# Performance work log

Hardware: AMD Instinct MI355X
Metric: run time of the kernel (lower is better)

Reference implementation:

```python
import jax, jax.numpy as jnp
from jax import lax
import numpy as np

BN_EPS = 1e-5


def setup_inputs() -> dict:
    key = jax.random.key(0)
    ks = jax.random.split(key, 10)
    B, S, I, H, O = 256, 2048, 64, 128, 1
    return {
        "x": jax.random.normal(ks[0], (B, S, I), dtype=jnp.float32),
        "mask": jax.random.randint(ks[1], (B, S, I), 0, 2, dtype=jnp.int32),
        "delta": jax.random.uniform(ks[2], (B, S, I), dtype=jnp.float32),
        "x_mean": jax.random.normal(ks[3], (I,), dtype=jnp.float32),
        "w_ih": jax.random.normal(ks[4], (3 * H, I), dtype=jnp.float32) * (1.0 / np.sqrt(H)),
        "w_hh": jax.random.normal(ks[5], (3 * H, H), dtype=jnp.float32) * (1.0 / np.sqrt(H)),
        "b_ih": jax.random.normal(ks[6], (3 * H,), dtype=jnp.float32) * 0.01,
        "b_hh": jax.random.normal(ks[7], (3 * H,), dtype=jnp.float32) * 0.01,
        "bn_gamma": jnp.ones((H,), dtype=jnp.float32),
        "bn_beta": jnp.zeros((H,), dtype=jnp.float32),
        "bn_mean": jnp.zeros((H,), dtype=jnp.float32),
        "bn_var": jnp.ones((H,), dtype=jnp.float32),
        "fc_w": jax.random.normal(ks[8], (O, H), dtype=jnp.float32) * (1.0 / np.sqrt(H)),
        "fc_b": jnp.zeros((O,), dtype=jnp.float32),
    }


def reference(x, mask, delta, x_mean, w_ih, w_hh, b_ih, b_hh,
              bn_gamma, bn_beta, bn_mean, bn_var, fc_w, fc_b):
    # delta is accepted by the torch module but unused in its forward.
    B, S, I = x.shape
    H = w_hh.shape[1]

    # --- last-observation-carry-forward imputation (scan over time) ---
    # After the per-step update, x_imputed[:, t] == last_obs, since
    # where(observed, x, last) followed by where(missing, last, x) == last.
    def impute_step(last, xm):
        xt, mt = xm  # [B, I], [B, I]
        last = jnp.where(mt > 0, xt, last)
        return last, last

    last0 = jnp.broadcast_to(x_mean, (B, I))
    x_t = jnp.transpose(x, (1, 0, 2))      # [S, B, I]
    m_t = jnp.transpose(mask, (1, 0, 2))   # [S, B, I]
    _, xi = lax.scan(impute_step, last0, (x_t, m_t))  # xi: [S, B, I]

    # --- single-layer GRU (PyTorch gate order: r, z, n) ---
    gates_x = jnp.einsum('sbi,gi->sbg', xi, w_ih) + b_ih  # [S, B, 3H]

    def gru_step(h, gx):
        gh = jnp.einsum('bh,gh->bg', h, w_hh) + b_hh  # [B, 3H]
        r = jax.nn.sigmoid(gx[:, :H] + gh[:, :H])
        z = jax.nn.sigmoid(gx[:, H:2 * H] + gh[:, H:2 * H])
        n = jnp.tanh(gx[:, 2 * H:] + r * gh[:, 2 * H:])
        h_new = (1.0 - z) * n + z * h
        return h_new, None

    h0 = jnp.zeros((B, H), dtype=x.dtype)
    h_last, _ = lax.scan(gru_step, h0, gates_x)  # [B, H]

    # --- dropout is identity in eval; BatchNorm1d in eval mode ---
    h_norm = (h_last - bn_mean) * lax.rsqrt(bn_var + BN_EPS) * bn_gamma + bn_beta

    return jnp.einsum('bh,oh->bo', h_norm, fc_w) + fc_b
```

## Files before the change

### kernel.cpp

```cpp
#include <hip/hip_runtime.h>
#include <cstddef>

#define SS 2048
#define BB 256
#define II 64
#define HH 128

typedef _Float16 h8 __attribute__((ext_vector_type(8)));
typedef _Float16 h2 __attribute__((ext_vector_type(2)));
typedef float    f4 __attribute__((ext_vector_type(4)));
typedef __fp16   fp16v2 __attribute__((ext_vector_type(2)));

__device__ __forceinline__ h2 pack_f16(float a, float b) {
  union { fp16v2 raw; h2 out; } cv;
  cv.raw = __builtin_amdgcn_cvt_pkrtz(a, b);
  return cv.out;
}
__device__ __forceinline__ float fast_rcp(float v) {
  return __builtin_amdgcn_rcpf(v);
}

#define KEEPA(x) asm volatile("" : "+a"(x))
#define KEEPV(x) asm volatile("" : "+v"(x))

__device__ __forceinline__ f4 mfma_first(const h8& a, const h8& b, const f4& c) {
  f4 d;
  asm volatile("v_mfma_f32_16x16x32_f16 %0, %1, %2, %3"
               : "=&v"(d) : "a"(a), "v"(b), "v"(c));
  return d;
}
__device__ __forceinline__ void mfma_acc(f4& d, const h8& a, const h8& b) {
  asm volatile("v_mfma_f32_16x16x32_f16 %0, %1, %2, %0"
               : "+v"(d) : "a"(a), "v"(b));
}

__device__ __forceinline__ void lds_barrier() {
  asm volatile("s_waitcnt lgkmcnt(0)" ::: "memory");
  __builtin_amdgcn_s_barrier();
}

__global__ __launch_bounds__(512) void gru_fused(
    const float* __restrict__ x,
    const int*   __restrict__ mask,
    const float* __restrict__ x_mean,
    const float* __restrict__ w_ih,
    const float* __restrict__ w_hh,
    const float* __restrict__ b_ih,
    const float* __restrict__ b_hh,
    const float* __restrict__ bn_gamma,
    const float* __restrict__ bn_beta,
    const float* __restrict__ bn_mean,
    const float* __restrict__ bn_var,
    const float* __restrict__ fc_w,
    const float* __restrict__ fc_b,
    float* __restrict__ out)
{
  const int b   = blockIdx.x;
  const int tid = threadIdx.x;
  const int wv  = tid >> 6;
  const int l   = tid & 63;
  const int col = l & 15;
  const int grp = l >> 4;

  __shared__ __align__(16) _Float16 h_lds[2][HH];
  __shared__ __align__(16) _Float16 xi_st[16][72];
  __shared__ __align__(16) float gx_lds[3][16][HH];
  __shared__ float h_fin[HH];

  h8 whA[3][4];
  h8 wiA[3][2];
  #pragma unroll
  for (int g = 0; g < 3; ++g) {
    const int row = g * HH + wv * 16 + col;
    #pragma unroll
    for (int kt = 0; kt < 4; ++kt) {
      const float* pw = w_hh + (size_t)row * HH + kt * 32 + grp * 8;
      float4 va = *reinterpret_cast<const float4*>(pw);
      float4 vb = *reinterpret_cast<const float4*>(pw + 4);
      h8 f;
      f[0]=(_Float16)va.x; f[1]=(_Float16)va.y; f[2]=(_Float16)va.z; f[3]=(_Float16)va.w;
      f[4]=(_Float16)vb.x; f[5]=(_Float16)vb.y; f[6]=(_Float16)vb.z; f[7]=(_Float16)vb.w;
      whA[g][kt] = f;
    }
    #pragma unroll
    for (int kt = 0; kt < 2; ++kt) {
      const float* pw = w_ih + (size_t)row * II + kt * 32 + grp * 8;
      float4 va = *reinterpret_cast<const float4*>(pw);
      float4 vb = *reinterpret_cast<const float4*>(pw + 4);
      h8 f;
      f[0]=(_Float16)va.x; f[1]=(_Float16)va.y; f[2]=(_Float16)va.z; f[3]=(_Float16)va.w;
      f[4]=(_Float16)vb.x; f[5]=(_Float16)vb.y; f[6]=(_Float16)vb.z; f[7]=(_Float16)vb.w;
      wiA[g][kt] = f;
    }
  }
  #pragma unroll
  for (int g = 0; g < 3; ++g) {
    #pragma unroll
    for (int kt = 0; kt < 4; ++kt) KEEPA(whA[g][kt]);
    #pragma unroll
    for (int kt = 0; kt < 2; ++kt) KEEPA(wiA[g][kt]);
  }

  f4 bRf, bZf, bNXf, bNHf;
  #pragma unroll
  for (int q = 0; q < 4; ++q) {
    const int hu = wv * 16 + grp * 4 + q;
    bRf[q]  = b_ih[hu]        + b_hh[hu];
    bZf[q]  = b_ih[HH + hu]   + b_hh[HH + hu];
    bNXf[q] = b_ih[2*HH + hu];
    bNHf[q] = b_hh[2*HH + hu];
  }
  f4 zf = {0.f, 0.f, 0.f, 0.f};
  KEEPV(bRf); KEEPV(bZf); KEEPV(bNXf); KEEPV(bNHf); KEEPV(zf);

  const int q_l  = col & 3;
  const int hu_l = wv * 16 + grp * 4 + q_l;
  const bool cs1 = (col & 1) != 0;
  const bool cs2 = (col & 2) != 0;
  const bool wlead = (col < 4);

  const size_t xbase = (size_t)b * SS * II;
  const float* xg = x + xbase;
  const int*   mg = mask + xbase;
  float last = 0.f;
  float x_stg[16];
  int   m_stg[16];
  if (tid < 64) {
    last = x_mean[tid];
    #pragma unroll
    for (int u = 0; u < 16; ++u) {
      x_stg[u] = xg[u * II + tid];
      m_stg[u] = mg[u * II + tid];
    }
  }
  float ho = 0.f;

  for (int gq = 0; gq < SS / 16; ++gq) {
    if (tid < 64) {
      #pragma unroll
      for (int u = 0; u < 16; ++u) {
        last = (m_stg[u] > 0) ? x_stg[u] : last;
        xi_st[u][tid] = pack_f16(last, last).x;
      }
      if (gq + 1 < SS / 16) {
        const float* xn = xg + (gq + 1) * 16 * II;
        const int*   mn = mg + (gq + 1) * 16 * II;
        #pragma unroll
        for (int u = 0; u < 16; ++u) {
          x_stg[u] = xn[u * II + tid];
          m_stg[u] = mn[u * II + tid];
        }
      }
    }
    lds_barrier();

    h8 xB0 = *reinterpret_cast<const h8*>(&xi_st[col][grp * 8]);
    h8 xB1 = *reinterpret_cast<const h8*>(&xi_st[col][32 + grp * 8]);
    f4 gR  = mfma_first(wiA[0][0], xB0, zf);
    f4 gZ  = mfma_first(wiA[1][0], xB0, zf);
    f4 gNX = mfma_first(wiA[2][0], xB0, bNXf);
    mfma_acc(gR,  wiA[0][1], xB1);
    mfma_acc(gZ,  wiA[1][1], xB1);
    mfma_acc(gNX, wiA[2][1], xB1);
    asm volatile("s_nop 7\n\ts_nop 7");
    __builtin_amdgcn_sched_barrier(0);
    *reinterpret_cast<f4*>(&gx_lds[0][col][wv * 16 + grp * 4]) = gR;
    *reinterpret_cast<f4*>(&gx_lds[1][col][wv * 16 + grp * 4]) = gZ;
    *reinterpret_cast<f4*>(&gx_lds[2][col][wv * 16 + grp * 4]) = gNX;

    #pragma unroll
    for (int tau = 0; tau < 16; ++tau) {
      const int p = tau & 1;
      if (wlead) h_lds[p][hu_l] = pack_f16(ho, ho).x;
      lds_barrier();

      h8 hB[4];
      #pragma unroll
      for (int kt = 0; kt < 4; ++kt)
        hB[kt] = *reinterpret_cast<const h8*>(&h_lds[p][kt * 32 + grp * 8]);

      f4 aR  = mfma_first(whA[0][0], hB[0], bRf);
      f4 aZ  = mfma_first(whA[1][0], hB[0], bZf);
      f4 aNH = mfma_first(whA[2][0], hB[0], bNHf);
      #pragma unroll
      for (int kt = 1; kt < 4; ++kt) {
        mfma_acc(aR,  whA[0][kt], hB[kt]);
        mfma_acc(aZ,  whA[1][kt], hB[kt]);
        mfma_acc(aNH, whA[2][kt], hB[kt]);
      }
      asm volatile("s_nop 7\n\ts_nop 7");
      __builtin_amdgcn_sched_barrier(0);

      const float gxR = gx_lds[0][tau][hu_l];
      const float gxZ = gx_lds[1][tau][hu_l];
      const float sNX = gx_lds[2][tau][hu_l];

      const float sR  = (cs2 ? (cs1 ? aR[3]  : aR[2])  : (cs1 ? aR[1]  : aR[0]))  + gxR;
      const float sZ  = (cs2 ? (cs1 ? aZ[3]  : aZ[2])  : (cs1 ? aZ[1]  : aZ[0]))  + gxZ;
      const float sNH =  cs2 ? (cs1 ? aNH[3] : aNH[2]) : (cs1 ? aNH[1] : aNH[0]);

      float r = fast_rcp(1.f + __expf(-sR));
      float z = fast_rcp(1.f + __expf(-sZ));
      float a = sNX + r * sNH;
      float n = 1.f - 2.f * fast_rcp(__expf(2.f * a) + 1.f);
      ho = n + z * (ho - n);
    }
  }

  if (wlead) h_fin[hu_l] = ho;
  __syncthreads();

  if (tid < 64) {
    float pacc = 0.f;
    #pragma unroll
    for (int q = 0; q < 2; ++q) {
      const int k = tid + q * 64;
      const float hv2 = h_fin[k];
      const float nrm = (hv2 - bn_mean[k]) * rsqrtf(bn_var[k] + 1e-5f) * bn_gamma[k] + bn_beta[k];
      pacc += nrm * fc_w[k];
    }
    #pragma unroll
    for (int off = 32; off > 0; off >>= 1) pacc += __shfl_down(pacc, off);
    if (tid == 0) out[b] = pacc + fc_b[0];
  }
}

extern "C" void kernel_launch(void* const* d_in, const int* in_sizes, int n_in,
                              void* d_out, int out_size, void* d_ws, size_t ws_size,
                              hipStream_t stream) {
  const float* x        = (const float*)d_in[0];
  const int*   mask     = (const int*)  d_in[1];
  const float* x_mean   = (const float*)d_in[3];
  const float* w_ih     = (const float*)d_in[4];
  const float* w_hh     = (const float*)d_in[5];
  const float* b_ih     = (const float*)d_in[6];
  const float* b_hh     = (const float*)d_in[7];
  const float* bn_gamma = (const float*)d_in[8];
  const float* bn_beta  = (const float*)d_in[9];
  const float* bn_mean  = (const float*)d_in[10];
  const float* bn_var   = (const float*)d_in[11];
  const float* fc_w     = (const float*)d_in[12];
  const float* fc_b     = (const float*)d_in[13];
  float* out = (float*)d_out;

  gru_fused<<<dim3(BB), dim3(512), 0, stream>>>(
      x, mask, x_mean, w_ih, w_hh, b_ih, b_hh,
      bn_gamma, bn_beta, bn_mean, bn_var, fc_w, fc_b, out);
}
```

Before: 823.8 us.

## Fold input-gate MFMA into first recurrent step and defer next-group prefetch

Moves the per-group input projection (xi × w_ih MFMAs) and its LDS store into the tau==0 iteration of the recurrent loop. This removes a separate barrier phase, so those MFMAs issue right after the recurrent MFMAs. The gx_lds layout is transposed to [gate][unit][17] with padding, so each wave writes and reads its own units and needs only a local waitcnt instead of a block barrier. The global prefetch of the next group's x/mask is moved after the first barrier so its latency overlaps compute. Correctness now depends on each wave reading only the gx entries it wrote itself.

```diff
diff --git a/kernel.cpp b/kernel.cpp
--- a/kernel.cpp
+++ b/kernel.cpp
@@ -5,6 +5,8 @@
 #define BB 256
 #define II 64
 #define HH 128
+#define GROUP 16
+#define NG (SS / GROUP)
 
 typedef _Float16 h8 __attribute__((ext_vector_type(8)));
 typedef _Float16 h2 __attribute__((ext_vector_type(2)));
@@ -63,8 +65,8 @@
   const int grp = l >> 4;
 
   __shared__ __align__(16) _Float16 h_lds[2][HH];
-  __shared__ __align__(16) _Float16 xi_st[16][72];
-  __shared__ __align__(16) float gx_lds[3][16][HH];
+  __shared__ __align__(16) _Float16 xi_st[GROUP][72];
+  __shared__ float gx_lds[3][HH][17];
   __shared__ float h_fin[HH];
 
   h8 whA[3][4];
@@ -118,6 +120,7 @@
   const bool cs1 = (col & 1) != 0;
   const bool cs2 = (col & 2) != 0;
   const bool wlead = (col < 4);
+  const int hub = wv * 16 + grp * 4;
 
   const size_t xbase = (size_t)b * SS * II;
   const float* xg = x + xbase;
@@ -128,51 +131,46 @@
   if (tid < 64) {
     last = x_mean[tid];
     #pragma unroll
-    for (int u = 0; u < 16; ++u) {
+    for (int u = 0; u < GROUP; ++u) {
       x_stg[u] = xg[u * II + tid];
       m_stg[u] = mg[u * II + tid];
     }
   }
   float ho = 0.f;
 
-  for (int gq = 0; gq < SS / 16; ++gq) {
+  for (int gq = 0; gq < NG; ++gq) {
     if (tid < 64) {
       #pragma unroll
-      for (int u = 0; u < 16; ++u) {
+      for (int u = 0; u < GROUP; ++u) {
         last = (m_stg[u] > 0) ? x_stg[u] : last;
         xi_st[u][tid] = pack_f16(last, last).x;
       }
-      if (gq + 1 < SS / 16) {
-        const float* xn = xg + (gq + 1) * 16 * II;
-        const int*   mn = mg + (gq + 1) * 16 * II;
-        #pragma unroll
-        for (int u = 0; u < 16; ++u) {
-          x_stg[u] = xn[u * II + tid];
-          m_stg[u] = mn[u * II + tid];
-        }
-      }
-    }
-    lds_barrier();
-
-    h8 xB0 = *reinterpret_cast<const h8*>(&xi_st[col][grp * 8]);
-    h8 xB1 = *reinterpret_cast<const h8*>(&xi_st[col][32 + grp * 8]);
-    f4 gR  = mfma_first(wiA[0][0], xB0, zf);
-    f4 gZ  = mfma_first(wiA[1][0], xB0, zf);
-    f4 gNX = mfma_first(wiA[2][0], xB0, bNXf);
-    mfma_acc(gR,  wiA[0][1], xB1);
-    mfma_acc(gZ,  wiA[1][1], xB1);
-    mfma_acc(gNX, wiA[2][1], xB1);
-    asm volatile("s_nop 7\n\ts_nop 7");
-    __builtin_amdgcn_sched_barrier(0);
-    *reinterpret_cast<f4*>(&gx_lds[0][col][wv * 16 + grp * 4]) = gR;
-    *reinterpret_cast<f4*>(&gx_lds[1][col][wv * 16 + grp * 4]) = gZ;
-    *reinterpret_cast<f4*>(&gx_lds[2][col][wv * 16 + grp * 4]) = gNX;
-
-    #pragma unroll
-    for (int tau = 0; tau < 16; ++tau) {
+    }
+
+    #pragma unroll
+    for (int tau = 0; tau < GROUP; ++tau) {
       const int p = tau & 1;
       if (wlead) h_lds[p][hu_l] = pack_f16(ho, ho).x;
       lds_barrier();
+
+      if (tau == 0) {
+        if (tid < 64 && gq + 1 < NG) {
+          const float* xn = xg + (size_t)(gq + 1) * GROUP * II;
+          const int*   mn = mg + (size_t)(gq + 1) * GROUP * II;
+          #pragma unroll
+          for (int u = 0; u < GROUP; ++u) {
+            x_stg[u] = xn[u * II + tid];
+            m_stg[u] = mn[u * II + tid];
+          }
+        }
+      }
+
+      float gxR, gxZ, sNX;
+      if (tau != 0) {
+        gxR = gx_lds[0][hu_l][tau];
+        gxZ = gx_lds[1][hu_l][tau];
+        sNX = gx_lds[2][hu_l][tau];
+      }
 
       h8 hB[4];
       #pragma unroll
@@ -188,12 +186,33 @@
         mfma_acc(aZ,  whA[1][kt], hB[kt]);
         mfma_acc(aNH, whA[2][kt], hB[kt]);
       }
-      asm volatile("s_nop 7\n\ts_nop 7");
-      __builtin_amdgcn_sched_barrier(0);
-
-      const float gxR = gx_lds[0][tau][hu_l];
-      const float gxZ = gx_lds[1][tau][hu_l];
-      const float sNX = gx_lds[2][tau][hu_l];
+
+      if (tau == 0) {
+        h8 xB0 = *reinterpret_cast<const h8*>(&xi_st[col][grp * 8]);
+        h8 xB1 = *reinterpret_cast<const h8*>(&xi_st[col][32 + grp * 8]);
+        f4 gR  = mfma_first(wiA[0][0], xB0, zf);
+        f4 gZ  = mfma_first(wiA[1][0], xB0, zf);
+        f4 gNX = mfma_first(wiA[2][0], xB0, bNXf);
+        mfma_acc(gR,  wiA[0][1], xB1);
+        mfma_acc(gZ,  wiA[1][1], xB1);
+        mfma_acc(gNX, wiA[2][1], xB1);
+        asm volatile("s_nop 7\n\ts_nop 7");
+        __builtin_amdgcn_sched_barrier(0);
+        #pragma unroll
+        for (int q = 0; q < 4; ++q) {
+          gx_lds[0][hub + q][col] = gR[q];
+          gx_lds[1][hub + q][col] = gZ[q];
+          gx_lds[2][hub + q][col] = gNX[q];
+        }
+        asm volatile("s_waitcnt lgkmcnt(0)" ::: "memory");
+        __builtin_amdgcn_sched_barrier(0);
+        gxR = gx_lds[0][hu_l][0];
+        gxZ = gx_lds[1][hu_l][0];
+        sNX = gx_lds[2][hu_l][0];
+      } else {
+        asm volatile("s_nop 7\n\ts_nop 7");
+        __builtin_amdgcn_sched_barrier(0);
+      }
 
       const float sR  = (cs2 ? (cs1 ? aR[3]  : aR[2])  : (cs1 ? aR[1]  : aR[0]))  + gxR;
       const float sZ  = (cs2 ? (cs1 ? aZ[3]  : aZ[2])  : (cs1 ? aZ[1]  : aZ[0]))  + gxZ;
```

Measured after the change: 756.1 us. 1.09x faster.
